# Kernel optimization log

Measured on AMD Instinct MI355X. Metric: run time of the kernel, lower is better.

## Reference

```python
import jax, jax.numpy as jnp
import numpy as np

ENT_GRID = 16
ENT_DIM = 64
N_RELATION = 5000
EMB_DIM = ENT_GRID * ENT_DIM  # 1024
BATCH = 8192
LN_EPS = 1e-5


def setup_inputs() -> dict:
    key = jax.random.key(0)
    k1, k2, k3, k4 = jax.random.split(key, 4)
    ent_emb = jax.random.normal(k1, (BATCH, EMB_DIM), dtype=jnp.float32)
    proj_ids = jax.random.randint(k2, (BATCH,), 0, N_RELATION, dtype=jnp.int64)
    # xavier_uniform for relation_tran: fan_in = fan_out treated over last two dims
    lim_t = float(np.sqrt(6.0 / (ENT_GRID + ENT_GRID)))
    relation_tran = jax.random.uniform(
        k3, (N_RELATION, ENT_DIM, ENT_GRID, ENT_GRID), jnp.float32, -lim_t, lim_t)
    lim_b = float(np.sqrt(6.0 / (ENT_DIM + ENT_GRID)))
    relation_bias = jax.random.uniform(
        k4, (N_RELATION, ENT_DIM, ENT_GRID), jnp.float32, -lim_b, lim_b)
    ln_weight = jnp.ones((EMB_DIM,), dtype=jnp.float32)
    ln_bias = jnp.zeros((EMB_DIM,), dtype=jnp.float32)
    return {
        "ent_emb": ent_emb,
        "proj_ids": proj_ids,
        "relation_tran": relation_tran,
        "relation_bias": relation_bias,
        "ln_weight": ln_weight,
        "ln_bias": ln_bias,
    }


def _layer_norm(x, w, b, eps=LN_EPS):
    mu = jnp.mean(x, axis=-1, keepdims=True)
    var = jnp.mean(jnp.square(x - mu), axis=-1, keepdims=True)
    return (x - mu) * jax.lax.rsqrt(var + eps) * w + b


def reference(ent_emb, proj_ids, relation_tran, relation_bias, ln_weight, ln_bias):
    B = ent_emb.shape[0]
    # gather per-query relation transform and bias
    rel_tran = relation_tran[proj_ids]  # (B, ent_dim, g, g)
    rel_bias = relation_bias[proj_ids]  # (B, ent_dim, g)
    # distribute: (B, emb_dim) -> (B, ent_dim, ent_grid); torch.chunk+stack == contiguous reshape
    e = ent_emb.reshape(B, ENT_DIM, ENT_GRID)
    # batched small matmul: (g,g) @ (g,) per (batch, ent_dim) block, plus bias
    x = jnp.einsum('bdgh,bdh->bdg', rel_tran, e) + rel_bias
    out = _layer_norm(x.reshape(B, EMB_DIM), ln_weight, ln_bias)
    return out
```

## Files before the change

### kernel.cpp

```cpp
#include <hip/hip_runtime.h>

#define ENT_GRID 16
#define ENT_DIM  64
#define EMB      1024
#define LN_EPS   1e-5f


__global__ void zero_hist_kernel(int* __restrict__ hist, int n) {
    int i = blockIdx.x * blockDim.x + threadIdx.x;
    if (i < n) hist[i] = 0;
}

__global__ void hist_kernel(const int* __restrict__ ids, int* __restrict__ hist, int B) {
    int i = blockIdx.x * blockDim.x + threadIdx.x;
    if (i < B) atomicAdd(&hist[ids[i]], 1);
}

__global__ __launch_bounds__(1024)
void scan_kernel(const int* __restrict__ hist, int* __restrict__ cursor, int n) {
    const int t = threadIdx.x;
    const int ITEMS = (n + 1023) / 1024;
    int vals[8];
    int lsum = 0;
#pragma unroll
    for (int k = 0; k < 8; ++k) {
        int i = t * ITEMS + k;
        int v = (k < ITEMS && i < n) ? hist[i] : 0;
        vals[k] = v;
        lsum += v;
    }
    __shared__ int s[1024];
    s[t] = lsum;
    __syncthreads();
    for (int off = 1; off < 1024; off <<= 1) {
        int v = (t >= off) ? s[t - off] : 0;
        __syncthreads();
        s[t] += v;
        __syncthreads();
    }
    int run = s[t] - lsum;
#pragma unroll
    for (int k = 0; k < 8; ++k) {
        int i = t * ITEMS + k;
        if (k < ITEMS && i < n) cursor[i] = run;
        run += vals[k];
    }
}

__global__ void scatter_kernel(const int* __restrict__ ids, int* __restrict__ cursor,
                               int* __restrict__ perm, int B) {
    int i = blockIdx.x * blockDim.x + threadIdx.x;
    if (i < B) {
        int pos = atomicAdd(&cursor[ids[i]], 1);
        perm[pos] = i;
    }
}

__global__ __launch_bounds__(256, 4)
void wproj_group_kernel(const float* __restrict__ ent_emb,
                        const float* __restrict__ rel_tran,
                        const float* __restrict__ rel_bias,
                        const float* __restrict__ ln_w,
                        const float* __restrict__ ln_b,
                        const int*   __restrict__ hist,
                        const int*   __restrict__ cursor_end,
                        const int*   __restrict__ perm,
                        float* __restrict__ out) {
    const int r   = blockIdx.x;
    const int cnt = hist[r];
    if (cnt == 0) return;
    const int start = cursor_end[r] - cnt;
    const int t = threadIdx.x;

    const float* __restrict__ tran = rel_tran + (size_t)r * (ENT_DIM * ENT_GRID * ENT_GRID);
    const float* __restrict__ bias = rel_bias + (size_t)r * (ENT_DIM * ENT_GRID);

    float4 trv[4][4];
    float  bias_v[4], lw[4], lb[4];
#pragma unroll
    for (int k = 0; k < 4; ++k) {
        const int i = t + k * 256;
        const float4* __restrict__ trp = reinterpret_cast<const float4*>(tran + (size_t)i * ENT_GRID);
#pragma unroll
        for (int q = 0; q < 4; ++q) trv[k][q] = trp[q];
        bias_v[k] = bias[i];
        lw[k] = ln_w[i];
        lb[k] = ln_b[i];
    }

    __shared__ float se[EMB];
    __shared__ float wsum[4], wsq[4];

    for (int j = 0; j < cnt; ++j) {
        const int b = perm[start + j];

        reinterpret_cast<float4*>(se)[t] =
            reinterpret_cast<const float4*>(ent_emb + (size_t)b * EMB)[t];
        __syncthreads();

        float x[4];
        float sum = 0.0f, sumsq = 0.0f;
#pragma unroll
        for (int k = 0; k < 4; ++k) {
            const int d = (t >> 4) + k * 16;
            const float4* __restrict__ er = reinterpret_cast<const float4*>(se + d * ENT_GRID);
            float acc = bias_v[k];
#pragma unroll
            for (int q = 0; q < 4; ++q) {
                float4 a  = trv[k][q];
                float4 ev = er[q];
                acc += a.x * ev.x + a.y * ev.y + a.z * ev.z + a.w * ev.w;
            }
            x[k]  = acc;
            sum   += acc;
            sumsq += acc * acc;
        }

#pragma unroll
        for (int off = 32; off > 0; off >>= 1) {
            sum   += __shfl_xor(sum, off, 64);
            sumsq += __shfl_xor(sumsq, off, 64);
        }
        const int wid = t >> 6;
        if ((t & 63) == 0) { wsum[wid] = sum; wsq[wid] = sumsq; }
        __syncthreads();

        const float tsum = wsum[0] + wsum[1] + wsum[2] + wsum[3];
        const float tsq  = wsq[0]  + wsq[1]  + wsq[2]  + wsq[3];
        const float mu   = tsum * (1.0f / (float)EMB);
        const float var  = tsq * (1.0f / (float)EMB) - mu * mu;
        const float rstd = rsqrtf(var + LN_EPS);

        float* __restrict__ ob = out + (size_t)b * EMB;
#pragma unroll
        for (int k = 0; k < 4; ++k) {
            const int i = t + k * 256;
            ob[i] = (x[k] - mu) * rstd * lw[k] + lb[k];
        }
        __syncthreads();
    }
}

extern "C" void kernel_launch(void* const* d_in, const int* in_sizes, int n_in,
                              void* d_out, int out_size, void* d_ws, size_t ws_size,
                              hipStream_t stream) {
    const float* ent_emb  = (const float*)d_in[0];
    const int*   proj_ids = (const int*)  d_in[1];
    const float* rel_tran = (const float*)d_in[2];
    const float* rel_bias = (const float*)d_in[3];
    const float* ln_w     = (const float*)d_in[4];
    const float* ln_b     = (const float*)d_in[5];
    float* out = (float*)d_out;

    const int B  = in_sizes[1];
    const int NR = in_sizes[2] / (ENT_DIM * ENT_GRID * ENT_GRID);

    int* w      = (int*)d_ws;
    int* hist   = w;
    int* cursor = w + NR;
    int* perm   = w + 2 * NR;

    zero_hist_kernel<<<(NR + 255) / 256, 256, 0, stream>>>(hist, NR);
    hist_kernel<<<(B + 255) / 256, 256, 0, stream>>>(proj_ids, hist, B);
    scan_kernel<<<1, 1024, 0, stream>>>(hist, cursor, NR);
    scatter_kernel<<<(B + 255) / 256, 256, 0, stream>>>(proj_ids, cursor, perm, B);

    wproj_group_kernel<<<NR, 256, 0, stream>>>(ent_emb, rel_tran, rel_bias, ln_w, ln_b,
                                               hist, cursor, perm, out);
}
```

Measured before the change: 90.51 us.

## Remap threads to contiguous outputs and batch four rows per sync

```diff
diff --git a/kernel.cpp b/kernel.cpp
--- a/kernel.cpp
+++ b/kernel.cpp
@@ -56,6 +56,10 @@
     }
 }
 
+__device__ __forceinline__ float dot4(float4 a, float4 b) {
+    return a.x * b.x + a.y * b.y + a.z * b.z + a.w * b.w;
+}
+
 __global__ __launch_bounds__(256, 4)
 void wproj_group_kernel(const float* __restrict__ ent_emb,
                         const float* __restrict__ rel_tran,
@@ -70,74 +74,81 @@
     const int cnt = hist[r];
     if (cnt == 0) return;
     const int start = cursor_end[r] - cnt;
-    const int t = threadIdx.x;
+    const int t   = threadIdx.x;
+    const int wid = t >> 6;
 
-    const float* __restrict__ tran = rel_tran + (size_t)r * (ENT_DIM * ENT_GRID * ENT_GRID);
-    const float* __restrict__ bias = rel_bias + (size_t)r * (ENT_DIM * ENT_GRID);
+    const float4* __restrict__ tr4 =
+        reinterpret_cast<const float4*>(rel_tran + (size_t)r * (ENT_DIM * ENT_GRID * ENT_GRID))
+        + (size_t)t * 16;
+    float4 trv[16];
+#pragma unroll
+    for (int q = 0; q < 16; ++q) trv[q] = tr4[q];
 
-    float4 trv[4][4];
-    float  bias_v[4], lw[4], lb[4];
+    const float4 bias4 = reinterpret_cast<const float4*>(rel_bias + (size_t)r * EMB)[t];
+    const float4 lw4   = reinterpret_cast<const float4*>(ln_w)[t];
+    const float4 lb4   = reinterpret_cast<const float4*>(ln_b)[t];
+
+    __shared__ float wsum[4][4], wsq[4][4];
+
+    for (int base = 0; base < cnt; base += 4) {
+        const int nrows = min(4, cnt - base);
+
+        int bidx[4];
 #pragma unroll
-    for (int k = 0; k < 4; ++k) {
-        const int i = t + k * 256;
-        const float4* __restrict__ trp = reinterpret_cast<const float4*>(tran + (size_t)i * ENT_GRID);
+        for (int j = 0; j < 4; ++j) {
+            const int jj = (j < nrows) ? j : (nrows - 1);
+            bidx[j] = perm[start + base + jj];
+        }
+
+        float x[4][4];
 #pragma unroll
-        for (int q = 0; q < 4; ++q) trv[k][q] = trp[q];
-        bias_v[k] = bias[i];
-        lw[k] = ln_w[i];
-        lb[k] = ln_b[i];
-    }
+        for (int j = 0; j < 4; ++j) {
+            if (j < nrows) {
+                const float4* __restrict__ e4 =
+                    reinterpret_cast<const float4*>(ent_emb + (size_t)bidx[j] * EMB)
+                    + (t >> 2) * 4;
+                const float4 ev0 = e4[0], ev1 = e4[1], ev2 = e4[2], ev3 = e4[3];
 
-    __shared__ float se[EMB];
-    __shared__ float wsum[4], wsq[4];
-
-    for (int j = 0; j < cnt; ++j) {
-        const int b = perm[start + j];
-
-        reinterpret_cast<float4*>(se)[t] =
-            reinterpret_cast<const float4*>(ent_emb + (size_t)b * EMB)[t];
+                float s = 0.0f, ss = 0.0f;
+#pragma unroll
+                for (int k = 0; k < 4; ++k) {
+                    float acc = (k == 0) ? bias4.x : (k == 1) ? bias4.y
+                              : (k == 2) ? bias4.z : bias4.w;
+                    acc += dot4(trv[k * 4 + 0], ev0);
+                    acc += dot4(trv[k * 4 + 1], ev1);
+                    acc += dot4(trv[k * 4 + 2], ev2);
+                    acc += dot4(trv[k * 4 + 3], ev3);
+                    x[j][k] = acc;
+                    s  += acc;
+                    ss += acc * acc;
+                }
+#pragma unroll
+                for (int off = 32; off > 0; off >>= 1) {
+                    s  += __shfl_xor(s, off, 64);
+                    ss += __shfl_xor(ss, off, 64);
+                }
+                if ((t & 63) == 0) { wsum[j][wid] = s; wsq[j][wid] = ss; }
+            }
+        }
         __syncthreads();
 
-        float x[4];
-        float sum = 0.0f, sumsq = 0.0f;
 #pragma unroll
-        for (int k = 0; k < 4; ++k) {
-            const int d = (t >> 4) + k * 16;
-            const float4* __restrict__ er = reinterpret_cast<const float4*>(se + d * ENT_GRID);
-            float acc = bias_v[k];
-#pragma unroll
-            for (int q = 0; q < 4; ++q) {
-                float4 a  = trv[k][q];
-                float4 ev = er[q];
-                acc += a.x * ev.x + a.y * ev.y + a.z * ev.z + a.w * ev.w;
+        for (int j = 0; j < 4; ++j) {
+            if (j < nrows) {
+                const float tsum = wsum[j][0] + wsum[j][1] + wsum[j][2] + wsum[j][3];
+                const float tsq  = wsq[j][0]  + wsq[j][1]  + wsq[j][2]  + wsq[j][3];
+                const float mu   = tsum * (1.0f / (float)EMB);
+                const float var  = tsq * (1.0f / (float)EMB) - mu * mu;
+                const float rstd = rsqrtf(var + LN_EPS);
+                float4 o;
+                o.x = (x[j][0] - mu) * rstd * lw4.x + lb4.x;
+                o.y = (x[j][1] - mu) * rstd * lw4.y + lb4.y;
+                o.z = (x[j][2] - mu) * rstd * lw4.z + lb4.z;
+                o.w = (x[j][3] - mu) * rstd * lw4.w + lb4.w;
+                reinterpret_cast<float4*>(out + (size_t)bidx[j] * EMB)[t] = o;
             }
-            x[k]  = acc;
-            sum   += acc;
-            sumsq += acc * acc;
         }
-
-#pragma unroll
-        for (int off = 32; off > 0; off >>= 1) {
-            sum   += __shfl_xor(sum, off, 64);
-            sumsq += __shfl_xor(sumsq, off, 64);
-        }
-        const int wid = t >> 6;
-        if ((t & 63) == 0) { wsum[wid] = sum; wsq[wid] = sumsq; }
-        __syncthreads();
-
-        const float tsum = wsum[0] + wsum[1] + wsum[2] + wsum[3];
-        const float tsq  = wsq[0]  + wsq[1]  + wsq[2]  + wsq[3];
-        const float mu   = tsum * (1.0f / (float)EMB);
-        const float var  = tsq * (1.0f / (float)EMB) - mu * mu;
-        const float rstd = rsqrtf(var + LN_EPS);
-
-        float* __restrict__ ob = out + (size_t)b * EMB;
-#pragma unroll
-        for (int k = 0; k < 4; ++k) {
-            const int i = t + k * 256;
-            ob[i] = (x[k] - mu) * rstd * lw[k] + lb[k];
-        }
-        __syncthreads();
+        if (base + 4 < cnt) __syncthreads();
     }
 }
 
```

Result: slower. 97.08 us (+7.3%).

## Use 1024-thread blocks with double-buffered rows and prefetch of the next embedding

Applied to the files above, without the earlier changes.

```diff
diff --git a/kernel.cpp b/kernel.cpp
--- a/kernel.cpp
+++ b/kernel.cpp
@@ -56,7 +56,11 @@
     }
 }
 
-__global__ __launch_bounds__(256, 4)
+__device__ __forceinline__ float dot4(float4 a, float4 b) {
+    return a.x * b.x + a.y * b.y + a.z * b.z + a.w * b.w;
+}
+
+__global__ __launch_bounds__(1024, 8)
 void wproj_group_kernel(const float* __restrict__ ent_emb,
                         const float* __restrict__ rel_tran,
                         const float* __restrict__ rel_bias,
@@ -71,73 +75,66 @@
     if (cnt == 0) return;
     const int start = cursor_end[r] - cnt;
     const int t = threadIdx.x;
+    const int w = t >> 6;
 
-    const float* __restrict__ tran = rel_tran + (size_t)r * (ENT_DIM * ENT_GRID * ENT_GRID);
-    const float* __restrict__ bias = rel_bias + (size_t)r * (ENT_DIM * ENT_GRID);
+    const float4* __restrict__ tr4 = reinterpret_cast<const float4*>(
+        rel_tran + (size_t)r * (ENT_DIM * ENT_GRID * ENT_GRID) + (size_t)t * ENT_GRID);
+    const float4 t0 = tr4[0], t1 = tr4[1], t2 = tr4[2], t3 = tr4[3];
+    const float bv  = rel_bias[(size_t)r * EMB + t];
+    const float lwv = ln_w[t];
+    const float lbv = ln_b[t];
 
-    float4 trv[4][4];
-    float  bias_v[4], lw[4], lb[4];
-#pragma unroll
-    for (int k = 0; k < 4; ++k) {
-        const int i = t + k * 256;
-        const float4* __restrict__ trp = reinterpret_cast<const float4*>(tran + (size_t)i * ENT_GRID);
-#pragma unroll
-        for (int q = 0; q < 4; ++q) trv[k][q] = trp[q];
-        bias_v[k] = bias[i];
-        lw[k] = ln_w[i];
-        lb[k] = ln_b[i];
-    }
+    __shared__ __align__(16) float se[2][EMB];
+    __shared__ __align__(16) float wred[2][2][16];
 
-    __shared__ float se[EMB];
-    __shared__ float wsum[4], wsq[4];
+    int   bcur = perm[start];
+    float vcur = ent_emb[(size_t)bcur * EMB + t];
 
     for (int j = 0; j < cnt; ++j) {
-        const int b = perm[start + j];
+        const int jb = j & 1;
+        se[jb][t] = vcur;
 
-        reinterpret_cast<float4*>(se)[t] =
-            reinterpret_cast<const float4*>(ent_emb + (size_t)b * EMB)[t];
-        __syncthreads();
-
-        float x[4];
-        float sum = 0.0f, sumsq = 0.0f;
-#pragma unroll
-        for (int k = 0; k < 4; ++k) {
-            const int d = (t >> 4) + k * 16;
-            const float4* __restrict__ er = reinterpret_cast<const float4*>(se + d * ENT_GRID);
-            float acc = bias_v[k];
-#pragma unroll
-            for (int q = 0; q < 4; ++q) {
-                float4 a  = trv[k][q];
-                float4 ev = er[q];
-                acc += a.x * ev.x + a.y * ev.y + a.z * ev.z + a.w * ev.w;
-            }
-            x[k]  = acc;
-            sum   += acc;
-            sumsq += acc * acc;
+        int bnext = 0; float vnext = 0.0f;
+        if (j + 1 < cnt) {
+            bnext = perm[start + j + 1];
+            vnext = ent_emb[(size_t)bnext * EMB + t];
         }
 
+        asm volatile("s_waitcnt lgkmcnt(0)\n\ts_barrier" ::: "memory");
+
+        const float4* __restrict__ er =
+            reinterpret_cast<const float4*>(&se[jb][(t >> 4) * ENT_GRID]);
+        const float x = bv + dot4(t0, er[0]) + dot4(t1, er[1])
+                           + dot4(t2, er[2]) + dot4(t3, er[3]);
+
+        float s = x, ss = x * x;
 #pragma unroll
         for (int off = 32; off > 0; off >>= 1) {
-            sum   += __shfl_xor(sum, off, 64);
-            sumsq += __shfl_xor(sumsq, off, 64);
+            s  += __shfl_xor(s, off, 64);
+            ss += __shfl_xor(ss, off, 64);
         }
-        const int wid = t >> 6;
-        if ((t & 63) == 0) { wsum[wid] = sum; wsq[wid] = sumsq; }
-        __syncthreads();
+        if ((t & 63) == 0) { wred[jb][0][w] = s; wred[jb][1][w] = ss; }
 
-        const float tsum = wsum[0] + wsum[1] + wsum[2] + wsum[3];
-        const float tsq  = wsq[0]  + wsq[1]  + wsq[2]  + wsq[3];
+        asm volatile("s_waitcnt lgkmcnt(0)\n\ts_barrier" ::: "memory");
+
+        float tsum = 0.0f, tsq = 0.0f;
+        const float4* __restrict__ ps = reinterpret_cast<const float4*>(&wred[jb][0][0]);
+        const float4* __restrict__ pq = reinterpret_cast<const float4*>(&wred[jb][1][0]);
+#pragma unroll
+        for (int q = 0; q < 4; ++q) {
+            const float4 a = ps[q];
+            const float4 c = pq[q];
+            tsum += a.x + a.y + a.z + a.w;
+            tsq  += c.x + c.y + c.z + c.w;
+        }
         const float mu   = tsum * (1.0f / (float)EMB);
         const float var  = tsq * (1.0f / (float)EMB) - mu * mu;
         const float rstd = rsqrtf(var + LN_EPS);
 
-        float* __restrict__ ob = out + (size_t)b * EMB;
-#pragma unroll
-        for (int k = 0; k < 4; ++k) {
-            const int i = t + k * 256;
-            ob[i] = (x[k] - mu) * rstd * lw[k] + lb[k];
-        }
-        __syncthreads();
+        out[(size_t)bcur * EMB + t] = (x - mu) * rstd * lwv + lbv;
+
+        bcur = bnext;
+        vcur = vnext;
     }
 }
 
@@ -165,6 +162,6 @@
     scan_kernel<<<1, 1024, 0, stream>>>(hist, cursor, NR);
     scatter_kernel<<<(B + 255) / 256, 256, 0, stream>>>(proj_ids, cursor, perm, B);
 
-    wproj_group_kernel<<<NR, 256, 0, stream>>>(ent_emb, rel_tran, rel_bias, ln_w, ln_b,
-                                               hist, cursor, perm, out);
+    wproj_group_kernel<<<NR, 1024, 0, stream>>>(ent_emb, rel_tran, rel_bias, ln_w, ln_b,
+                                                hist, cursor, perm, out);
 }
```

After: 100.1 us. 1.11x slower.
